# Kernel tuning notes

Hardware: AMD Instinct MI355X
Metric: run time of the kernel (lower is better)

The kernel has to match this reference:

```python
import jax, jax.numpy as jnp
import numpy as np

H = 4          # number of GCN heads (hard-coded self.h = 4)
EPS = 1e-6     # MWPToolkit LayerNorm eps
B, K, D, HID = 16, 1024, 256, 256
DK = D // H


def setup_inputs() -> dict:
    key = jax.random.key(0)
    ks = jax.random.split(key, 12)
    sc = lambda fan_in: 1.0 / np.sqrt(fan_in).astype(np.float32)
    return {
        "graph_nodes": jax.random.normal(ks[0], (B, K, D), jnp.float32),
        "graph": jax.random.randint(ks[1], (B, 5, K, K), 0, 2, jnp.int32),
        # per-head GCN layer 1: GraphConvolution(indim -> hiddim)
        "Wg1": jax.random.normal(ks[2], (H, D, HID), jnp.float32) * sc(D),
        "bg1": jax.random.normal(ks[3], (H, HID), jnp.float32) * sc(D),
        # per-head GCN layer 2: GraphConvolution(hiddim -> d_k)
        "Wg2": jax.random.normal(ks[4], (H, HID, DK), jnp.float32) * sc(HID),
        "bg2": jax.random.normal(ks[5], (H, DK), jnp.float32) * sc(HID),
        # PositionwiseFeedForward: Linear(indim,hiddim) -> ReLU -> Linear(hiddim,outdim)
        "Wf1": jax.random.normal(ks[6], (D, HID), jnp.float32) * sc(D),
        "bf1": jax.random.normal(ks[7], (HID,), jnp.float32) * sc(D),
        "Wf2": jax.random.normal(ks[8], (HID, D), jnp.float32) * sc(HID),
        "bf2": jax.random.normal(ks[9], (D,), jnp.float32) * sc(HID),
        # LayerNorm(outdim) affine params
        "ln_a": jnp.ones((D,), jnp.float32),
        "ln_b": jnp.zeros((D,), jnp.float32),
    }


def reference(graph_nodes, graph, Wg1, bg1, Wg2, bg2, Wf1, bf1, Wf2, bf2, ln_a, ln_b):
    adj = graph.astype(jnp.float32)                      # (B, 5, K, K)
    # adj_list = [adj[:,1], adj[:,1], adj[:,4], adj[:,4]] -> stack heads
    adj_h = jnp.stack([adj[:, 1], adj[:, 1], adj[:, 4], adj[:, 4]])  # (H,B,K,K)

    # GCN layer 1 (all heads at once): relu(adj @ (x @ W1) + b1)
    sup1 = jnp.einsum('bkd,hdf->hbkf', graph_nodes, Wg1)            # (H,B,K,HID)
    h1 = jax.nn.relu(jnp.einsum('hbkj,hbjf->hbkf', adj_h, sup1)
                     + bg1[:, None, None, :])
    # (dropout is identity in eval)
    # GCN layer 2: adj @ (h1 @ W2) + b2
    sup2 = jnp.einsum('hbkf,hfe->hbke', h1, Wg2)                    # (H,B,K,DK)
    h2 = jnp.einsum('hbkj,hbje->hbke', adj_h, sup2) + bg2[:, None, None, :]

    # concat heads along feature dim: (B,K,H*DK) == (B,K,D)
    g = jnp.transpose(h2, (1, 2, 0, 3)).reshape(h2.shape[1], h2.shape[2], -1)

    # MWPToolkit LayerNorm: a*(x-mean)/(std+eps)+b, std unbiased (ddof=1)
    mu = g.mean(-1, keepdims=True)
    sd = jnp.std(g, axis=-1, keepdims=True, ddof=1)
    g = ln_a * (g - mu) / (sd + EPS) + ln_b + graph_nodes           # residual

    # PositionwiseFeedForward + residual (dropout identity in eval)
    ff = jax.nn.relu(g @ Wf1 + bf1) @ Wf2 + bf2
    out = ff + g
    return adj, out
```

## Files before the change

kernel.cpp:

```cpp
#include <hip/hip_runtime.h>

typedef unsigned short ushort_t;
using short8  = __attribute__((ext_vector_type(8))) short;
using floatx4 = __attribute__((ext_vector_type(4))) float;

__device__ __forceinline__ ushort_t f2bf(float f) {
  unsigned int x = __builtin_bit_cast(unsigned int, f);
  x += 0x7fffu + ((x >> 16) & 1u);
  return (ushort_t)(x >> 16);
}

__device__ __forceinline__ void gld16(const ushort_t* g, ushort_t* l) {
  __builtin_amdgcn_global_load_lds(
      (const __attribute__((address_space(1))) void*)(unsigned long long)(uintptr_t)g,
      (__attribute__((address_space(3))) void*)l, 16, 0, 0);
}

template <typename F>
__device__ __forceinline__ void gemm_tile(const ushort_t* __restrict__ A, int lda,
                                          const ushort_t* __restrict__ BT, int ldb,
                                          int K, F epi) {
  __shared__ ushort_t As[128 * 64];
  __shared__ ushort_t Bs[128 * 64];

  const int tid  = threadIdx.x;
  const int wave = tid >> 6;
  const int lane = tid & 63;
  const int l15  = lane & 15;
  const int quad = lane >> 4;
  const int wm   = wave >> 1;
  const int wn   = wave & 1;

  const int srow8  = lane >> 3;
  const int schunk = lane & 7;
  const int gcol   = ((schunk ^ srow8) * 8);

  const ushort_t* gA = A  + (size_t)(wave * 32 + srow8) * lda + gcol;
  const ushort_t* gB = BT + (size_t)(wave * 32 + srow8) * ldb + gcol;
  ushort_t* lA = As + (wave * 32) * 64;
  ushort_t* lB = Bs + (wave * 32) * 64;

  floatx4 acc[4][4] = {};

  const int arow0 = (wm * 64 + l15) * 64;
  const int brow0 = (wn * 64 + l15) * 64;
  const int cx    = l15 & 7;

  for (int k0 = 0; k0 < K; k0 += 64) {
#pragma unroll
    for (int ci = 0; ci < 4; ci++) {
      gld16(gA + (size_t)(ci * 8) * lda, lA + ci * 512);
      gld16(gB + (size_t)(ci * 8) * ldb, lB + ci * 512);
    }
    gA += 64; gB += 64;
    __syncthreads();
#pragma unroll
    for (int ks = 0; ks < 2; ks++) {
      const int cs = ((ks * 4 + quad) ^ cx) * 8;
      short8 af[4], bfr[4];
#pragma unroll
      for (int i = 0; i < 4; i++) af[i]  = *(const short8*)(As + arow0 + i * 1024 + cs);
#pragma unroll
      for (int j = 0; j < 4; j++) bfr[j] = *(const short8*)(Bs + brow0 + j * 1024 + cs);
#pragma unroll
      for (int i = 0; i < 4; i++)
#pragma unroll
        for (int j = 0; j < 4; j++)
          acc[i][j] = __builtin_amdgcn_mfma_f32_16x16x32_bf16(af[i], bfr[j], acc[i][j], 0, 0, 0);
    }
    __syncthreads();
  }

#pragma unroll
  for (int i = 0; i < 4; i++)
#pragma unroll
    for (int j = 0; j < 4; j++)
#pragma unroll
      for (int r = 0; r < 4; r++)
        epi(wm * 64 + i * 16 + quad * 4 + r, wn * 64 + j * 16 + l15, acc[i][j][r]);
}


__global__ __launch_bounds__(256) void k_adjb(const int* __restrict__ graph,
                                              ushort_t* __restrict__ adjb) {
  const size_t i = (size_t)blockIdx.x * 256 + threadIdx.x;
  const size_t e0 = i * 4;
  const unsigned bt = (unsigned)(e0 >> 20);
  const unsigned b = bt >> 1, t = bt & 1;
  const unsigned s = t ? 4u : 1u;
  int4 v = *(const int4*)(graph + (((size_t)(b * 5 + s)) << 20) + (e0 & 0xFFFFFu));
  ushort4 h;
  h.x = f2bf((float)v.x); h.y = f2bf((float)v.y);
  h.z = f2bf((float)v.z); h.w = f2bf((float)v.w);
  *(ushort4*)(adjb + e0) = h;
}

__global__ __launch_bounds__(256) void k_adjf32(const int* __restrict__ graph,
                                                float* __restrict__ adj_out) {
  const size_t i = (size_t)blockIdx.x * 256 + threadIdx.x;
  int4 v = ((const int4*)graph)[i];
  ((float4*)adj_out)[i] = make_float4((float)v.x, (float)v.y, (float)v.z, (float)v.w);
}

__global__ __launch_bounds__(256) void k_xt(const float* __restrict__ gn,
                                            ushort_t* __restrict__ XT) {
  __shared__ float t[64][68];
  const int b = blockIdx.z, dt = blockIdx.y, kt = blockIdx.x;
  const int r  = threadIdx.x >> 4;
  const int c4 = (threadIdx.x & 15) * 4;
#pragma unroll
  for (int rr = 0; rr < 4; rr++) {
    const int kl = rr * 16 + r;
    float4 v = *(const float4*)(gn + ((size_t)(b * 1024 + kt * 64 + kl)) * 256 + dt * 64 + c4);
    t[kl][c4] = v.x; t[kl][c4 + 1] = v.y; t[kl][c4 + 2] = v.z; t[kl][c4 + 3] = v.w;
  }
  __syncthreads();
#pragma unroll
  for (int rr = 0; rr < 4; rr++) {
    const int dl = rr * 16 + r;
    ushort4 h;
    h.x = f2bf(t[c4][dl]);     h.y = f2bf(t[c4 + 1][dl]);
    h.z = f2bf(t[c4 + 2][dl]); h.w = f2bf(t[c4 + 3][dl]);
    *(ushort4*)(XT + ((size_t)(b * 256 + dt * 64 + dl)) * 1024 + kt * 64 + c4) = h;
  }
}

__global__ __launch_bounds__(256) void k_prepw(const float* __restrict__ Wg1, const float* __restrict__ Wg2,
                                               const float* __restrict__ Wf1, const float* __restrict__ Wf2,
                                               ushort_t* __restrict__ W1T, ushort_t* __restrict__ Wg2bd,
                                               ushort_t* __restrict__ Wf1T, ushort_t* __restrict__ Wf2T) {
  const int i = blockIdx.x * 256 + threadIdx.x;
  if (i < 262144) {
    const int fI = i >> 8, d = i & 255;
    const int h = fI >> 8, ff = fI & 255;
    W1T[i] = f2bf(Wg1[((h << 8) + d) * 256 + ff]);
  } else if (i < 524288) {
    const int j = i - 262144;
    const int r = j >> 10, c = j & 1023;
    const int h = r >> 6, e = r & 63;
    const float v = ((c >> 8) == h) ? Wg2[((h << 8) + (c & 255)) * 64 + e] : 0.f;
    Wg2bd[j] = f2bf(v);
  } else if (i < 589824) {
    const int j = i - 524288;
    const int n = j >> 8, k = j & 255;
    Wf1T[j] = f2bf(Wf1[k * 256 + n]);
  } else if (i < 655360) {
    const int j = i - 589824;
    const int n = j >> 8, k = j & 255;
    Wf2T[j] = f2bf(Wf2[k * 256 + n]);
  }
}


__global__ __launch_bounds__(256) void k_ax(const ushort_t* __restrict__ adjb,
                                            const ushort_t* __restrict__ XT,
                                            ushort_t* __restrict__ AX) {
  const int nt = blockIdx.x, mt = blockIdx.y, bt = blockIdx.z;
  const int b = bt >> 1;
  const ushort_t* A  = adjb + ((size_t)bt << 20) + (size_t)mt * 128 * 1024;
  const ushort_t* BT = XT + ((size_t)b << 18) + (size_t)nt * 128 * 1024;
  ushort_t* C = AX + ((size_t)bt << 18);
  gemm_tile(A, 1024, BT, 1024, 1024, [&](int r, int c, float v) {
    C[(size_t)(mt * 128 + r) * 256 + nt * 128 + c] = f2bf(v);
  });
}

__global__ __launch_bounds__(256) void k_h1(const ushort_t* __restrict__ AX,
                                            const ushort_t* __restrict__ W1T,
                                            const float* __restrict__ bg1,
                                            ushort_t* __restrict__ h1) {
  const int nt = blockIdx.x, mt = blockIdx.y, b = blockIdx.z;
  const int t = nt >> 2;
  const ushort_t* A  = AX + ((size_t)(b * 2 + t) << 18) + (size_t)mt * 128 * 256;
  const ushort_t* BT = W1T + (size_t)nt * 128 * 256;
  ushort_t* C = h1 + ((size_t)b << 20);
  const float* bias = bg1 + nt * 128;
  gemm_tile(A, 256, BT, 256, 256, [&](int r, int c, float v) {
    C[(size_t)(mt * 128 + r) * 1024 + nt * 128 + c] = f2bf(fmaxf(v + bias[c], 0.f));
  });
}

__global__ __launch_bounds__(256) void k_g3(const ushort_t* __restrict__ Wg2bd,
                                            const ushort_t* __restrict__ h1,
                                            ushort_t* __restrict__ sup2T) {
  const int nt = blockIdx.x, mt = blockIdx.y, b = blockIdx.z;
  const ushort_t* A  = Wg2bd + (size_t)mt * 128 * 1024;
  const ushort_t* BT = h1 + ((size_t)b << 20) + (size_t)nt * 128 * 1024;
  ushort_t* C = sup2T + (size_t)b * 262144;
  gemm_tile(A, 1024, BT, 1024, 1024, [&](int r, int c, float v) {
    C[(size_t)(mt * 128 + r) * 1024 + nt * 128 + c] = f2bf(v);
  });
}

__global__ __launch_bounds__(256) void k_g4(const ushort_t* __restrict__ adjb,
                                            const ushort_t* __restrict__ sup2T,
                                            const float* __restrict__ bg2,
                                            float* __restrict__ g) {
  const int nt = blockIdx.x, mt = blockIdx.y, b = blockIdx.z;
  const ushort_t* A  = adjb + ((size_t)(b * 2 + nt) << 20) + (size_t)mt * 128 * 1024;
  const ushort_t* BT = sup2T + (size_t)b * 262144 + (size_t)nt * 128 * 1024;
  float* C = g + (size_t)b * 262144;
  const float* bias = bg2 + nt * 128;
  gemm_tile(A, 1024, BT, 1024, 1024, [&](int r, int c, float v) {
    C[(size_t)(mt * 128 + r) * 256 + nt * 128 + c] = v + bias[c];
  });
}

__global__ __launch_bounds__(256) void k_ln(const float* __restrict__ g, const float* __restrict__ gn,
                                            const float* __restrict__ la, const float* __restrict__ lb,
                                            float* __restrict__ glnf, ushort_t* __restrict__ glnb) {
  const int row = blockIdx.x * 4 + (threadIdx.x >> 6);
  const int lane = threadIdx.x & 63;
  const float4 x = ((const float4*)(g + (size_t)row * 256))[lane];
  float s = x.x + x.y + x.z + x.w;
#pragma unroll
  for (int o = 1; o < 64; o <<= 1) s += __shfl_xor(s, o);
  const float mu = s * (1.f / 256.f);
  const float dx = x.x - mu, dy = x.y - mu, dz = x.z - mu, dw = x.w - mu;
  float q = dx * dx + dy * dy + dz * dz + dw * dw;
#pragma unroll
  for (int o = 1; o < 64; o <<= 1) q += __shfl_xor(q, o);
  const float inv = 1.f / (sqrtf(q * (1.f / 255.f)) + 1e-6f);
  const float4 a  = ((const float4*)la)[lane];
  const float4 bb = ((const float4*)lb)[lane];
  const float4 rz = ((const float4*)(gn + (size_t)row * 256))[lane];
  float4 o;
  o.x = a.x * dx * inv + bb.x + rz.x;
  o.y = a.y * dy * inv + bb.y + rz.y;
  o.z = a.z * dz * inv + bb.z + rz.z;
  o.w = a.w * dw * inv + bb.w + rz.w;
  ((float4*)(glnf + (size_t)row * 256))[lane] = o;
  ushort4 h; h.x = f2bf(o.x); h.y = f2bf(o.y); h.z = f2bf(o.z); h.w = f2bf(o.w);
  ((ushort4*)(glnb + (size_t)row * 256))[lane] = h;
}

__global__ __launch_bounds__(256) void k_f1(const ushort_t* __restrict__ gln,
                                            const ushort_t* __restrict__ Wf1T,
                                            const float* __restrict__ bf1,
                                            ushort_t* __restrict__ tb) {
  const int nt = blockIdx.x, mt = blockIdx.y;
  const ushort_t* A  = gln + (size_t)mt * 128 * 256;
  const ushort_t* BT = Wf1T + (size_t)nt * 128 * 256;
  const float* bias = bf1 + nt * 128;
  gemm_tile(A, 256, BT, 256, 256, [&](int r, int c, float v) {
    tb[(size_t)(mt * 128 + r) * 256 + nt * 128 + c] = f2bf(fmaxf(v + bias[c], 0.f));
  });
}

__global__ __launch_bounds__(256) void k_f2(const ushort_t* __restrict__ tb,
                                            const ushort_t* __restrict__ Wf2T,
                                            const float* __restrict__ bf2,
                                            const float* __restrict__ glnf,
                                            float* __restrict__ out) {
  const int nt = blockIdx.x, mt = blockIdx.y;
  const ushort_t* A  = tb + (size_t)mt * 128 * 256;
  const ushort_t* BT = Wf2T + (size_t)nt * 128 * 256;
  const float* bias = bf2 + nt * 128;
  gemm_tile(A, 256, BT, 256, 256, [&](int r, int c, float v) {
    const size_t idx = (size_t)(mt * 128 + r) * 256 + nt * 128 + c;
    out[idx] = v + bias[c] + glnf[idx];
  });
}

extern "C" void kernel_launch(void* const* d_in, const int* in_sizes, int n_in,
                              void* d_out, int out_size, void* d_ws, size_t ws_size,
                              hipStream_t stream) {
  const float* gnodes = (const float*)d_in[0];
  const int*   graph  = (const int*)d_in[1];
  const float* Wg1 = (const float*)d_in[2];
  const float* bg1 = (const float*)d_in[3];
  const float* Wg2 = (const float*)d_in[4];
  const float* bg2 = (const float*)d_in[5];
  const float* Wf1 = (const float*)d_in[6];
  const float* bf1 = (const float*)d_in[7];
  const float* Wf2 = (const float*)d_in[8];
  const float* bf2 = (const float*)d_in[9];
  const float* ln_a = (const float*)d_in[10];
  const float* ln_b = (const float*)d_in[11];

  float* adj_out = (float*)d_out;
  float* out     = (float*)d_out + 83886080;

  char* ws = (char*)d_ws;
  ushort_t* adjb  = (ushort_t*)(ws);
  ushort_t* XT    = (ushort_t*)(ws + 67108864);
  ushort_t* W1T   = (ushort_t*)(ws + 75497472);
  ushort_t* Wg2bd = (ushort_t*)(ws + 76021760);
  ushort_t* Wf1T  = (ushort_t*)(ws + 76546048);
  ushort_t* Wf2T  = (ushort_t*)(ws + 76677120);
  ushort_t* AX    = (ushort_t*)(ws + 76808192);
  ushort_t* h1    = (ushort_t*)(ws + 93585408);
  ushort_t* sup2T = (ushort_t*)(ws + 127139840);
  float*    gbuf  = (float*)(ws + 135528448);
  float*    glnf  = (float*)(ws + 152305664);
  ushort_t* glnb  = (ushort_t*)(ws + 169082880);
  ushort_t* tbuf  = (ushort_t*)(ws + 177471488);

  k_adjb <<<32768, 256, 0, stream>>>(graph, adjb);
  k_xt   <<<dim3(16, 4, 16), 256, 0, stream>>>(gnodes, XT);
  k_prepw<<<2560, 256, 0, stream>>>(Wg1, Wg2, Wf1, Wf2, W1T, Wg2bd, Wf1T, Wf2T);

  k_ax<<<dim3(2, 8, 32), 256, 0, stream>>>(adjb, XT, AX);
  k_h1<<<dim3(8, 8, 16), 256, 0, stream>>>(AX, W1T, bg1, h1);
  k_g3<<<dim3(8, 2, 16), 256, 0, stream>>>(Wg2bd, h1, sup2T);
  k_g4<<<dim3(2, 8, 16), 256, 0, stream>>>(adjb, sup2T, bg2, gbuf);

  k_ln<<<4096, 256, 0, stream>>>(gbuf, gnodes, ln_a, ln_b, glnf, glnb);

  k_f1<<<dim3(2, 128), 256, 0, stream>>>(glnb, Wf1T, bf1, tbuf);
  k_f2<<<dim3(2, 128), 256, 0, stream>>>(tbuf, Wf2T, bf2, glnf, out);

  k_adjf32<<<81920, 256, 0, stream>>>(graph, adj_out);
}
```

Baseline: 720.8 us.

## Fuse adjacency casts, widen GEMM tiles, and drop zero blocks in layer-2 weight GEMM

```diff
diff --git a/kernel.cpp b/kernel.cpp
--- a/kernel.cpp
+++ b/kernel.cpp
@@ -41,7 +41,6 @@
   ushort_t* lB = Bs + (wave * 32) * 64;
 
   floatx4 acc[4][4] = {};
-
   const int arow0 = (wm * 64 + l15) * 64;
   const int brow0 = (wn * 64 + l15) * 64;
   const int cx    = l15 & 7;
@@ -80,26 +79,87 @@
         epi(wm * 64 + i * 16 + quad * 4 + r, wn * 64 + j * 16 + l15, acc[i][j][r]);
 }
 
-
-__global__ __launch_bounds__(256) void k_adjb(const int* __restrict__ graph,
+template <typename F>
+__device__ __forceinline__ void gemm_tile_w(const ushort_t* __restrict__ A, int lda,
+                                            const ushort_t* __restrict__ BT, int ldb,
+                                            int K, F epi) {
+  __shared__ ushort_t As[128 * 64];
+  __shared__ ushort_t Bs[256 * 64];
+
+  const int tid  = threadIdx.x;
+  const int wave = tid >> 6;
+  const int lane = tid & 63;
+  const int l15  = lane & 15;
+  const int quad = lane >> 4;
+  const int wm   = wave >> 2;
+  const int wn   = wave & 3;
+
+  const int srow8  = lane >> 3;
+  const int schunk = lane & 7;
+  const int gcol   = ((schunk ^ srow8) * 8);
+
+  const ushort_t* gA = A  + (size_t)(wave * 16 + srow8) * lda + gcol;
+  const ushort_t* gB = BT + (size_t)(wave * 32 + srow8) * ldb + gcol;
+  ushort_t* lA = As + (wave * 16) * 64;
+  ushort_t* lB = Bs + (wave * 32) * 64;
+
+  floatx4 acc[4][4] = {};
+  const int arow0 = (wm * 64 + l15) * 64;
+  const int brow0 = (wn * 64 + l15) * 64;
+  const int cx    = l15 & 7;
+
+  for (int k0 = 0; k0 < K; k0 += 64) {
+#pragma unroll
+    for (int ci = 0; ci < 2; ci++)
+      gld16(gA + (size_t)(ci * 8) * lda, lA + ci * 512);
+#pragma unroll
+    for (int ci = 0; ci < 4; ci++)
+      gld16(gB + (size_t)(ci * 8) * ldb, lB + ci * 512);
+    gA += 64; gB += 64;
+    __syncthreads();
+#pragma unroll
+    for (int ks = 0; ks < 2; ks++) {
+      const int cs = ((ks * 4 + quad) ^ cx) * 8;
+      short8 af[4], bfr[4];
+#pragma unroll
+      for (int i = 0; i < 4; i++) af[i]  = *(const short8*)(As + arow0 + i * 1024 + cs);
+#pragma unroll
+      for (int j = 0; j < 4; j++) bfr[j] = *(const short8*)(Bs + brow0 + j * 1024 + cs);
+#pragma unroll
+      for (int i = 0; i < 4; i++)
+#pragma unroll
+        for (int j = 0; j < 4; j++)
+          acc[i][j] = __builtin_amdgcn_mfma_f32_16x16x32_bf16(af[i], bfr[j], acc[i][j], 0, 0, 0);
+    }
+    __syncthreads();
+  }
+
+#pragma unroll
+  for (int i = 0; i < 4; i++)
+#pragma unroll
+    for (int j = 0; j < 4; j++)
+#pragma unroll
+      for (int r = 0; r < 4; r++)
+        epi(wm * 64 + i * 16 + quad * 4 + r, wn * 64 + j * 16 + l15, acc[i][j][r]);
+}
+
+
+__global__ __launch_bounds__(256) void k_cast(const int* __restrict__ graph,
+                                              float* __restrict__ adj_out,
                                               ushort_t* __restrict__ adjb) {
   const size_t i = (size_t)blockIdx.x * 256 + threadIdx.x;
+  int4 v = ((const int4*)graph)[i];
+  float4 f = make_float4((float)v.x, (float)v.y, (float)v.z, (float)v.w);
+  ((float4*)adj_out)[i] = f;
   const size_t e0 = i * 4;
-  const unsigned bt = (unsigned)(e0 >> 20);
-  const unsigned b = bt >> 1, t = bt & 1;
-  const unsigned s = t ? 4u : 1u;
-  int4 v = *(const int4*)(graph + (((size_t)(b * 5 + s)) << 20) + (e0 & 0xFFFFFu));
-  ushort4 h;
-  h.x = f2bf((float)v.x); h.y = f2bf((float)v.y);
-  h.z = f2bf((float)v.z); h.w = f2bf((float)v.w);
-  *(ushort4*)(adjb + e0) = h;
-}
-
-__global__ __launch_bounds__(256) void k_adjf32(const int* __restrict__ graph,
-                                                float* __restrict__ adj_out) {
-  const size_t i = (size_t)blockIdx.x * 256 + threadIdx.x;
-  int4 v = ((const int4*)graph)[i];
-  ((float4*)adj_out)[i] = make_float4((float)v.x, (float)v.y, (float)v.z, (float)v.w);
+  const unsigned sb = (unsigned)(e0 >> 20);
+  const unsigned s = sb % 5u, b = sb / 5u;
+  if (s == 1u || s == 4u) {
+    const unsigned tt = (s == 4u) ? 1u : 0u;
+    ushort4 h;
+    h.x = f2bf(f.x); h.y = f2bf(f.y); h.z = f2bf(f.z); h.w = f2bf(f.w);
+    *(ushort4*)(adjb + (((size_t)(b * 2 + tt)) << 20) + (e0 & 0xFFFFFu)) = h;
+  }
 }
 
 __global__ __launch_bounds__(256) void k_xt(const float* __restrict__ gn,
@@ -127,68 +187,71 @@
 
 __global__ __launch_bounds__(256) void k_prepw(const float* __restrict__ Wg1, const float* __restrict__ Wg2,
                                                const float* __restrict__ Wf1, const float* __restrict__ Wf2,
-                                               ushort_t* __restrict__ W1T, ushort_t* __restrict__ Wg2bd,
+                                               ushort_t* __restrict__ W1T, ushort_t* __restrict__ W2pT,
                                                ushort_t* __restrict__ Wf1T, ushort_t* __restrict__ Wf2T) {
   const int i = blockIdx.x * 256 + threadIdx.x;
   if (i < 262144) {
     const int fI = i >> 8, d = i & 255;
     const int h = fI >> 8, ff = fI & 255;
     W1T[i] = f2bf(Wg1[((h << 8) + d) * 256 + ff]);
-  } else if (i < 524288) {
+  } else if (i < 393216) {
     const int j = i - 262144;
-    const int r = j >> 10, c = j & 1023;
-    const int h = r >> 6, e = r & 63;
-    const float v = ((c >> 8) == h) ? Wg2[((h << 8) + (c & 255)) * 64 + e] : 0.f;
-    Wg2bd[j] = f2bf(v);
-  } else if (i < 589824) {
-    const int j = i - 524288;
+    const int t = j >> 16, rem = j & 65535;
+    const int ep = rem >> 9, k = rem & 511;
+    const int hh = ep >> 6;
+    const float v = ((k >> 8) == hh)
+        ? Wg2[(((t * 2 + hh) << 8) + (k & 255)) * 64 + (ep & 63)] : 0.f;
+    W2pT[j] = f2bf(v);
+  } else if (i < 458752) {
+    const int j = i - 393216;
     const int n = j >> 8, k = j & 255;
     Wf1T[j] = f2bf(Wf1[k * 256 + n]);
-  } else if (i < 655360) {
-    const int j = i - 589824;
+  } else if (i < 524288) {
+    const int j = i - 458752;
     const int n = j >> 8, k = j & 255;
     Wf2T[j] = f2bf(Wf2[k * 256 + n]);
   }
 }
 
 
-__global__ __launch_bounds__(256) void k_ax(const ushort_t* __restrict__ adjb,
+__global__ __launch_bounds__(512) void k_ax(const ushort_t* __restrict__ adjb,
                                             const ushort_t* __restrict__ XT,
                                             ushort_t* __restrict__ AX) {
-  const int nt = blockIdx.x, mt = blockIdx.y, bt = blockIdx.z;
+  const int mt = blockIdx.x, bt = blockIdx.y;
   const int b = bt >> 1;
   const ushort_t* A  = adjb + ((size_t)bt << 20) + (size_t)mt * 128 * 1024;
-  const ushort_t* BT = XT + ((size_t)b << 18) + (size_t)nt * 128 * 1024;
+  const ushort_t* BT = XT + ((size_t)b << 18);
   ushort_t* C = AX + ((size_t)bt << 18);
-  gemm_tile(A, 1024, BT, 1024, 1024, [&](int r, int c, float v) {
-    C[(size_t)(mt * 128 + r) * 256 + nt * 128 + c] = f2bf(v);
-  });
-}
-
-__global__ __launch_bounds__(256) void k_h1(const ushort_t* __restrict__ AX,
+  gemm_tile_w(A, 1024, BT, 1024, 1024, [&](int r, int c, float v) {
+    C[(size_t)(mt * 128 + r) * 256 + c] = f2bf(v);
+  });
+}
+
+__global__ __launch_bounds__(512) void k_h1(const ushort_t* __restrict__ AX,
                                             const ushort_t* __restrict__ W1T,
                                             const float* __restrict__ bg1,
                                             ushort_t* __restrict__ h1) {
   const int nt = blockIdx.x, mt = blockIdx.y, b = blockIdx.z;
-  const int t = nt >> 2;
+  const int t = nt >> 1;
   const ushort_t* A  = AX + ((size_t)(b * 2 + t) << 18) + (size_t)mt * 128 * 256;
-  const ushort_t* BT = W1T + (size_t)nt * 128 * 256;
+  const ushort_t* BT = W1T + ((size_t)nt << 16);
   ushort_t* C = h1 + ((size_t)b << 20);
-  const float* bias = bg1 + nt * 128;
-  gemm_tile(A, 256, BT, 256, 256, [&](int r, int c, float v) {
-    C[(size_t)(mt * 128 + r) * 1024 + nt * 128 + c] = f2bf(fmaxf(v + bias[c], 0.f));
-  });
-}
-
-__global__ __launch_bounds__(256) void k_g3(const ushort_t* __restrict__ Wg2bd,
+  const float* bias = bg1 + nt * 256;
+  gemm_tile_w(A, 256, BT, 256, 256, [&](int r, int c, float v) {
+    C[(size_t)(mt * 128 + r) * 1024 + nt * 256 + c] = f2bf(fmaxf(v + bias[c], 0.f));
+  });
+}
+
+__global__ __launch_bounds__(256) void k_g3(const ushort_t* __restrict__ W2pT,
                                             const ushort_t* __restrict__ h1,
                                             ushort_t* __restrict__ sup2T) {
-  const int nt = blockIdx.x, mt = blockIdx.y, b = blockIdx.z;
-  const ushort_t* A  = Wg2bd + (size_t)mt * 128 * 1024;
-  const ushort_t* BT = h1 + ((size_t)b << 20) + (size_t)nt * 128 * 1024;
-  ushort_t* C = sup2T + (size_t)b * 262144;
-  gemm_tile(A, 1024, BT, 1024, 1024, [&](int r, int c, float v) {
-    C[(size_t)(mt * 128 + r) * 1024 + nt * 128 + c] = f2bf(v);
+  const int nt = blockIdx.x, bt = blockIdx.y;
+  const int b = bt >> 1, t = bt & 1;
+  const ushort_t* A  = W2pT + (size_t)t * 65536;
+  const ushort_t* BT = h1 + ((size_t)b << 20) + (size_t)nt * 131072 + t * 512;
+  ushort_t* C = sup2T + (size_t)bt * 131072;
+  gemm_tile(A, 512, BT, 1024, 512, [&](int r, int c, float v) {
+    C[(size_t)r * 1024 + nt * 128 + c] = f2bf(v);
   });
 }
 
@@ -198,7 +261,7 @@
                                             float* __restrict__ g) {
   const int nt = blockIdx.x, mt = blockIdx.y, b = blockIdx.z;
   const ushort_t* A  = adjb + ((size_t)(b * 2 + nt) << 20) + (size_t)mt * 128 * 1024;
-  const ushort_t* BT = sup2T + (size_t)b * 262144 + (size_t)nt * 128 * 1024;
+  const ushort_t* BT = sup2T + (size_t)(b * 2 + nt) * 131072;
   float* C = g + (size_t)b * 262144;
   const float* bias = bg2 + nt * 128;
   gemm_tile(A, 1024, BT, 1024, 1024, [&](int r, int c, float v) {
@@ -285,30 +348,28 @@
   ushort_t* adjb  = (ushort_t*)(ws);
   ushort_t* XT    = (ushort_t*)(ws + 67108864);
   ushort_t* W1T   = (ushort_t*)(ws + 75497472);
-  ushort_t* Wg2bd = (ushort_t*)(ws + 76021760);
-  ushort_t* Wf1T  = (ushort_t*)(ws + 76546048);
-  ushort_t* Wf2T  = (ushort_t*)(ws + 76677120);
-  ushort_t* AX    = (ushort_t*)(ws + 76808192);
-  ushort_t* h1    = (ushort_t*)(ws + 93585408);
-  ushort_t* sup2T = (ushort_t*)(ws + 127139840);
-  float*    gbuf  = (float*)(ws + 135528448);
-  float*    glnf  = (float*)(ws + 152305664);
-  ushort_t* glnb  = (ushort_t*)(ws + 169082880);
-  ushort_t* tbuf  = (ushort_t*)(ws + 177471488);
-
-  k_adjb <<<32768, 256, 0, stream>>>(graph, adjb);
+  ushort_t* W2pT  = (ushort_t*)(ws + 76021760);
+  ushort_t* Wf1T  = (ushort_t*)(ws + 76283904);
+  ushort_t* Wf2T  = (ushort_t*)(ws + 76414976);
+  ushort_t* AX    = (ushort_t*)(ws + 76546048);
+  ushort_t* h1    = (ushort_t*)(ws + 93323264);
+  ushort_t* sup2T = (ushort_t*)(ws + 126877696);
+  float*    gbuf  = (float*)(ws + 135266304);
+  float*    glnf  = (float*)(ws + 152043520);
+  ushort_t* glnb  = (ushort_t*)(ws + 168820736);
+  ushort_t* tbuf  = (ushort_t*)(ws + 177209344);
+
   k_xt   <<<dim3(16, 4, 16), 256, 0, stream>>>(gnodes, XT);
-  k_prepw<<<2560, 256, 0, stream>>>(Wg1, Wg2, Wf1, Wf2, W1T, Wg2bd, Wf1T, Wf2T);
-
-  k_ax<<<dim3(2, 8, 32), 256, 0, stream>>>(adjb, XT, AX);
-  k_h1<<<dim3(8, 8, 16), 256, 0, stream>>>(AX, W1T, bg1, h1);
-  k_g3<<<dim3(8, 2, 16), 256, 0, stream>>>(Wg2bd, h1, sup2T);
+  k_prepw<<<2048, 256, 0, stream>>>(Wg1, Wg2, Wf1, Wf2, W1T, W2pT, Wf1T, Wf2T);
+  k_cast <<<81920, 256, 0, stream>>>(graph, adj_out, adjb);
+
+  k_ax<<<dim3(8, 32), 512, 0, stream>>>(adjb, XT, AX);
+  k_h1<<<dim3(4, 8, 16), 512, 0, stream>>>(AX, W1T, bg1, h1);
+  k_g3<<<dim3(8, 32), 256, 0, stream>>>(W2pT, h1, sup2T);
   k_g4<<<dim3(2, 8, 16), 256, 0, stream>>>(adjb, sup2T, bg2, gbuf);
 
   k_ln<<<4096, 256, 0, stream>>>(gbuf, gnodes, ln_a, ln_b, glnf, glnb);
 
   k_f1<<<dim3(2, 128), 256, 0, stream>>>(glnb, Wf1T, bf1, tbuf);
   k_f2<<<dim3(2, 128), 256, 0, stream>>>(tbuf, Wf2T, bf2, glnf, out);
-
-  k_adjf32<<<81920, 256, 0, stream>>>(graph, adj_out);
-}
+}
```

Result: no change. 712.6 us (-1.1%).
